# Performance work log

Hardware: AMD Instinct MI355X
Metric: run time of the kernel (lower is better)

Reference implementation:

```python
import jax, jax.numpy as jnp
import numpy as np
import math

B, NG, LS, E = 2, 8, 512, 1024
NH = 16
HD = E // NH
EPS = 1e-6


def rms_norm(x, w):
    xf = x.astype(jnp.float32)
    n = xf * jax.lax.rsqrt(jnp.mean(xf * xf, axis=-1, keepdims=True) + EPS)
    return n.astype(x.dtype) * w


def rotate(x):
    # pairs (a,b) -> (-b, a), matching view(...,-1,2).flip(-1); x[...,0]*=-1
    x2 = x.reshape(*x.shape[:-1], HD // 2, 2)
    out = jnp.stack([-x2[..., 1], x2[..., 0]], axis=-1)
    return out.reshape(x.shape)


def setup_inputs() -> dict:
    key = jax.random.key(0)
    k1, k2, k3 = jax.random.split(key, 3)
    x = jax.random.normal(k1, (B, NG, LS, E), dtype=jnp.float32)
    W_qkv = jax.random.normal(k2, (E, 3 * E), dtype=jnp.float32) * (1.0 / math.sqrt(E))
    ln_w = jnp.ones((E,), dtype=jnp.float32)
    W_proj = jax.random.normal(k3, (E, E), dtype=jnp.float32) * (1.0 / math.sqrt(E))
    return {"x": x, "W_qkv": W_qkv, "ln_w": ln_w, "W_proj": W_proj}


def reference(x, W_qkv, ln_w, W_proj):
    b, ng, ls, _ = x.shape
    qkv = jnp.einsum('bgsc,ce->bgse', x, W_qkv)  # fused QKV projection
    q, k, v = jnp.split(qkv, 3, axis=-1)
    # QK RMSNorm over full embedding dim (before head split)
    q = rms_norm(q, ln_w)
    k = rms_norm(k, ln_w)
    # [B, ng, nh, ls, hd]
    q = q.reshape(b, ng, ls, NH, HD).swapaxes(2, 3)
    k = k.reshape(b, ng, ls, NH, HD).swapaxes(2, 3)
    v = v.reshape(b, ng, ls, NH, HD).swapaxes(2, 3)
    # RoPE (repo's variant: angles duplicated across halves, adjacent-pair rotate)
    pos = 10000.0 ** ((-2.0 * jnp.arange(0, HD, 2, dtype=jnp.float32) - 1.0) / HD)
    token_seq = jnp.arange(ls, dtype=jnp.float32)[:, None] * pos[None, :]  # [ls, hd/2]
    rot = jnp.concatenate([token_seq, token_seq], axis=-1)  # [ls, hd]
    cos, sin = jnp.cos(rot), jnp.sin(rot)
    q = q * cos + rotate(q) * sin
    k = k * cos + rotate(k) * sin
    # causal attention, scale = 1/sqrt(head_dim) (muP=False)
    scale = 1.0 / math.sqrt(HD)
    scores = jnp.einsum('bgnqd,bgnkd->bgnqk', q, k) * scale
    causal = jnp.tril(jnp.ones((ls, ls), dtype=bool))
    scores = jnp.where(causal, scores, jnp.finfo(scores.dtype).min)
    att = jax.nn.softmax(scores, axis=-1)
    y = jnp.einsum('bgnqk,bgnkd->bgnqd', att, v)
    y = y.swapaxes(2, 3).reshape(b, ng, ls, E)
    y = jnp.einsum('bgse,ef->bgsf', y, W_proj)
    return y
```

## Files before the change

kernel.cpp:

```cpp
#include <hip/hip_runtime.h>

typedef unsigned short u16;
typedef unsigned int   u32;
typedef __attribute__((ext_vector_type(8))) short bf16x8;
typedef __attribute__((ext_vector_type(4))) float f32x4;

#define MFMA16(a,b,c) __builtin_amdgcn_mfma_f32_16x16x32_bf16((a),(b),(c),0,0,0)
#define GLD16(gp, lp) __builtin_amdgcn_global_load_lds((const __attribute__((address_space(1))) u32*)(gp), (__attribute__((address_space(3))) u32*)(lp), 16, 0, 0)

#define B_   2
#define NG_  8
#define LS_  512
#define E_   1024
#define NH_  16
#define HD_  64
#define NTOK 8192

__device__ __forceinline__ u16 f2bu(float f){
  u32 u = __builtin_bit_cast(u32, f);
  u32 r = u + 0x7FFFu + ((u >> 16) & 1u);
  return (u16)(r >> 16);
}
__device__ __forceinline__ float b2f(u16 h){
  u32 u = ((u32)h) << 16;
  return __builtin_bit_cast(float, u);
}
__device__ __forceinline__ u32 pk2(float lo, float hi){
  u32 r; asm("v_cvt_pk_bf16_f32 %0, %1, %2" : "=v"(r) : "v"(lo), "v"(hi)); return r;
}

__global__ __launch_bounds__(256) void k_conv_x(const float* __restrict__ x, u16* __restrict__ xb){
  int i = blockIdx.x * 256 + threadIdx.x;
  float4 v = ((const float4*)x)[i];
  ((ushort4*)xb)[i] = make_ushort4(f2bu(v.x), f2bu(v.y), f2bu(v.z), f2bu(v.w));
}

__global__ __launch_bounds__(256) void k_transpose(const float* __restrict__ W, u16* __restrict__ WT,
                                                   int Kd, int Nd){
  __shared__ float tile[32][33];
  int tx = threadIdx.x & 31, ty = threadIdx.x >> 5;
  int c0 = blockIdx.x * 32, r0 = blockIdx.y * 32;
  #pragma unroll
  for (int i = 0; i < 4; i++)
    tile[ty + i*8][tx] = W[(size_t)(r0 + ty + i*8) * Nd + c0 + tx];
  __syncthreads();
  #pragma unroll
  for (int i = 0; i < 4; i++)
    WT[(size_t)(c0 + ty + i*8) * Kd + r0 + tx] = f2bu(tile[tx][ty + i*8]);
}

__global__ __launch_bounds__(256) void k_rope_table(float* __restrict__ ct, float* __restrict__ st){
  int i = blockIdx.x * 256 + threadIdx.x;
  int s = i >> 6, d = i & 63, j = d & 31;
  float freq = powf(10000.f, -(4.f * (float)j + 1.f) / 64.f);
  float th = (float)s * freq;
  ct[i] = cosf(th);
  st[i] = sinf(th);
}

template <typename OutT, bool FUSE_VT>
__global__ __launch_bounds__(256, 2) void k_gemm_bt(const u16* __restrict__ A, const u16* __restrict__ Bt,
                                                    OutT* __restrict__ C, u16* __restrict__ vt,
                                                    int M, int N, int K){
  int nbn = N >> 7;
  int cpx = gridDim.x >> 3;
  int bid = (blockIdx.x & 7) * cpx + (blockIdx.x >> 3);
  int tm = bid / nbn, tn = bid % nbn;
  int tid = threadIdx.x;
  int w = tid >> 6, l = tid & 63;
  int lr = l & 15, lg = l >> 4;
  int wm = (w >> 1) * 64, wn = (w & 1) * 64;

  __shared__ u16 smem[2][2][128 * 64];

  const u16* Ab = A  + (size_t)(tm * 128) * K;
  const u16* Bb = Bt + (size_t)(tn * 128) * K;
  int NT = K >> 6;

  int srow0 = tid >> 3, ssl = tid & 7;
  auto stage = [&](int t, int s){
    int k0 = t << 6;
    #pragma unroll
    for (int q = 0; q < 4; q++){
      int row = q * 32 + srow0;
      int sc  = (ssl ^ (row & 7)) << 3;
      GLD16(Ab + (size_t)row * K + k0 + sc, &smem[s][0][q * 2048 + tid * 8]);
    }
    #pragma unroll
    for (int q = 0; q < 4; q++){
      int row = q * 32 + srow0;
      int sc  = (ssl ^ (row & 7)) << 3;
      GLD16(Bb + (size_t)row * K + k0 + sc, &smem[s][1][q * 2048 + tid * 8]);
    }
  };

  f32x4 acc[4][4] = {};

  stage(0, 0);
  stage(1, 1);
  asm volatile("s_waitcnt vmcnt(8)" ::: "memory");
  asm volatile("s_barrier" ::: "memory");

  for (int t = 0; t < NT; t++){
    int s = t & 1;
    const u16* As = smem[s][0];
    const u16* Bs = smem[s][1];
    bf16x8 bfr[4][2], afr[2][2];
    #pragma unroll
    for (int j = 0; j < 4; j++){
      int rb = wn + j * 16 + lr;
      #pragma unroll
      for (int kk = 0; kk < 2; kk++)
        bfr[j][kk] = *(const bf16x8*)&Bs[rb * 64 + ((kk * 32 + lg * 8) ^ ((rb & 7) << 3))];
    }
    #pragma unroll
    for (int i = 0; i < 2; i++){
      int ra = wm + i * 16 + lr;
      #pragma unroll
      for (int kk = 0; kk < 2; kk++)
        afr[i][kk] = *(const bf16x8*)&As[ra * 64 + ((kk * 32 + lg * 8) ^ ((ra & 7) << 3))];
    }
    __builtin_amdgcn_s_setprio(1);
    #pragma unroll
    for (int i = 0; i < 2; i++)
      #pragma unroll
      for (int j = 0; j < 4; j++){
        acc[i][j] = MFMA16(afr[i][0], bfr[j][0], acc[i][j]);
        acc[i][j] = MFMA16(afr[i][1], bfr[j][1], acc[i][j]);
      }
    __builtin_amdgcn_s_setprio(0);
    asm volatile("s_barrier" ::: "memory");
    #pragma unroll
    for (int i = 0; i < 2; i++){
      int ra = wm + (i + 2) * 16 + lr;
      #pragma unroll
      for (int kk = 0; kk < 2; kk++)
        afr[i][kk] = *(const bf16x8*)&As[ra * 64 + ((kk * 32 + lg * 8) ^ ((ra & 7) << 3))];
    }
    __builtin_amdgcn_s_setprio(1);
    #pragma unroll
    for (int i = 0; i < 2; i++)
      #pragma unroll
      for (int j = 0; j < 4; j++){
        acc[i + 2][j] = MFMA16(afr[i][0], bfr[j][0], acc[i + 2][j]);
        acc[i + 2][j] = MFMA16(afr[i][1], bfr[j][1], acc[i + 2][j]);
      }
    __builtin_amdgcn_s_setprio(0);
    asm volatile("s_barrier" ::: "memory");
    if (t + 2 < NT){
      stage(t + 2, s);
      asm volatile("s_waitcnt vmcnt(8)" ::: "memory");
      asm volatile("s_barrier" ::: "memory");
    } else if (t + 2 == NT){
      asm volatile("s_waitcnt vmcnt(0)" ::: "memory");
      asm volatile("s_barrier" ::: "memory");
    }
  }

  if constexpr (FUSE_VT){
    if (tn >= 16){
      int h  = (tn - 16) * 2 + (wn >> 6);
      int bg = tm >> 2;
      u16* vbase = vt + (size_t)(bg * 16 + h) * HD_ * LS_;
      #pragma unroll
      for (int i = 0; i < 4; i++){
        int s0 = (tm & 3) * 128 + wm + i * 16 + lg * 4;
        #pragma unroll
        for (int j = 0; j < 4; j++){
          int d = j * 16 + lr;
          ushort4 pk = make_ushort4(f2bu(acc[i][j][0]), f2bu(acc[i][j][1]),
                                    f2bu(acc[i][j][2]), f2bu(acc[i][j][3]));
          *(ushort4*)&vbase[(size_t)d * LS_ + s0] = pk;
        }
      }
      return;
    }
  }

  #pragma unroll
  for (int i = 0; i < 4; i++)
    #pragma unroll
    for (int j = 0; j < 4; j++)
      #pragma unroll
      for (int r = 0; r < 4; r++){
        int row = tm * 128 + wm + i * 16 + lg * 4 + r;
        int col = tn * 128 + wn + j * 16 + lr;
        float v = acc[i][j][r];
        if constexpr (sizeof(OutT) == 2) C[(size_t)row * N + col] = f2bu(v);
        else                             C[(size_t)row * N + col] = v;
      }
}

__global__ __launch_bounds__(256) void k_norm_rope(const u16* __restrict__ qkv, const float* __restrict__ lnw,
                                                   const float* __restrict__ ct, const float* __restrict__ st,
                                                   u16* __restrict__ qh, u16* __restrict__ kh){
  int tok = blockIdx.x;
  int t = threadIdx.x;
  int s = tok & (LS_ - 1);
  int bg = tok >> 9;
  const u16* row = qkv + (size_t)tok * 3072;
  int e0 = t * 4;

  ushort4 q4 = *(const ushort4*)&row[e0];
  ushort4 k4 = *(const ushort4*)&row[1024 + e0];
  float qf[4] = {b2f(q4.x), b2f(q4.y), b2f(q4.z), b2f(q4.w)};
  float kf[4] = {b2f(k4.x), b2f(k4.y), b2f(k4.z), b2f(k4.w)};

  float qss = 0.f, kss = 0.f;
  #pragma unroll
  for (int j = 0; j < 4; j++){ qss += qf[j]*qf[j]; kss += kf[j]*kf[j]; }
  #pragma unroll
  for (int o = 32; o; o >>= 1){ qss += __shfl_down(qss, o); kss += __shfl_down(kss, o); }
  __shared__ float redq[4], redk[4];
  if ((t & 63) == 0){ redq[t >> 6] = qss; redk[t >> 6] = kss; }
  __syncthreads();
  float qsum = redq[0] + redq[1] + redq[2] + redq[3];
  float ksum = redk[0] + redk[1] + redk[2] + redk[3];
  float qr = rsqrtf(qsum * (1.f / 1024.f) + 1e-6f);
  float kr = rsqrtf(ksum * (1.f / 1024.f) + 1e-6f);

  float qn[4], kn[4];
  #pragma unroll
  for (int j = 0; j < 4; j++){
    float wv = lnw[e0 + j];
    qn[j] = qf[j] * qr * wv;
    kn[j] = kf[j] * kr * wv;
  }
  int d0 = e0 & 63, h = e0 >> 6;
  const float* cr = ct + s * 64 + d0;
  const float* sr = st + s * 64 + d0;
  float qo[4], ko[4];
  #pragma unroll
  for (int p = 0; p < 4; p += 2){
    float c0 = cr[p], s0 = sr[p], c1 = cr[p+1], s1 = sr[p+1];
    qo[p]   = qn[p]   * c0 - qn[p+1] * s0;
    qo[p+1] = qn[p+1] * c1 + qn[p]   * s1;
    ko[p]   = kn[p]   * c0 - kn[p+1] * s0;
    ko[p+1] = kn[p+1] * c1 + kn[p]   * s1;
  }
  size_t oidx = (((size_t)bg * NH_ + h) * LS_ + s) * HD_ + d0;
  *(ushort4*)&qh[oidx] = make_ushort4(f2bu(qo[0]*0.125f), f2bu(qo[1]*0.125f), f2bu(qo[2]*0.125f), f2bu(qo[3]*0.125f));
  *(ushort4*)&kh[oidx] = make_ushort4(f2bu(ko[0]), f2bu(ko[1]), f2bu(ko[2]), f2bu(ko[3]));
}

__global__ __launch_bounds__(64) void k_attn(const u16* __restrict__ qh, const u16* __restrict__ kh,
                                             const u16* __restrict__ vt, u16* __restrict__ ytok){
  int bid = blockIdx.x;
  int head = bid & 255;
  int j = 15 - (bid >> 8);
  int l = threadIdx.x & 63;
  int lr = l & 15, lg = l >> 4;
  int q0 = j * 32;
  int ntw = (j >> 1) + 1;

  const u16* Qp = qh + (size_t)head * LS_ * HD_;
  const u16* Kp = kh + (size_t)head * LS_ * HD_;
  const u16* Vp = vt + (size_t)head * HD_ * LS_;
  int bg = head >> 4, h = head & 15;
  u16* Yb = ytok + (size_t)bg * LS_ * E_ + h * HD_;

  bf16x8 aq[2][2];
  #pragma unroll
  for (int mi = 0; mi < 2; mi++)
    #pragma unroll
    for (int kk = 0; kk < 2; kk++)
      aq[mi][kk] = *(const bf16x8*)&Qp[(q0 + mi*16 + lr) * 64 + kk * 32 + lg * 8];

  __shared__ u16 Pw[32 * 72];

  f32x4 o[2][4] = {};
  float mrun[2] = {-1e30f, -1e30f}, lrun[2] = {0.f, 0.f};

  bf16x8 kr[4][2];
  auto loadK = [&](int kv0){
    #pragma unroll
    for (int nk = 0; nk < 4; nk++){
      kr[nk][0] = *(const bf16x8*)&Kp[(kv0 + nk*16 + lr) * 64 + lg * 8];
      kr[nk][1] = *(const bf16x8*)&Kp[(kv0 + nk*16 + lr) * 64 + 32 + lg * 8];
    }
  };
  loadK(0);

  for (int tkv = 0; tkv < ntw; tkv++){
    int kv0 = tkv * 64;
    f32x4 sa[2][4] = {};
    __builtin_amdgcn_s_setprio(1);
    #pragma unroll
    for (int nk = 0; nk < 4; nk++)
      #pragma unroll
      for (int mi = 0; mi < 2; mi++){
        sa[mi][nk] = MFMA16(kr[nk][0], aq[mi][0], sa[mi][nk]);
        sa[mi][nk] = MFMA16(kr[nk][1], aq[mi][1], sa[mi][nk]);
      }
    __builtin_amdgcn_s_setprio(0);
    if (tkv + 1 < ntw) loadK(kv0 + 64);
    bf16x8 vr[4][2];
    #pragma unroll
    for (int nd = 0; nd < 4; nd++){
      vr[nd][0] = *(const bf16x8*)&Vp[(nd*16 + lr) * 512 + kv0 + lg * 8];
      vr[nd][1] = *(const bf16x8*)&Vp[(nd*16 + lr) * 512 + kv0 + 32 + lg * 8];
    }
    if (kv0 + 63 > q0){
      #pragma unroll
      for (int mi = 0; mi < 2; mi++){
        int qg = q0 + mi*16 + lr;
        #pragma unroll
        for (int nk = 0; nk < 4; nk++)
          #pragma unroll
          for (int r = 0; r < 4; r++){
            int kg = kv0 + nk*16 + lg*4 + r;
            if (kg > qg) sa[mi][nk][r] = -1e30f;
          }
      }
    }
    float pmax[2];
    #pragma unroll
    for (int mi = 0; mi < 2; mi++){
      float pm = sa[mi][0][0];
      #pragma unroll
      for (int nk = 0; nk < 4; nk++)
        #pragma unroll
        for (int r = 0; r < 4; r++) pm = fmaxf(pm, sa[mi][nk][r]);
      pm = fmaxf(pm, __shfl_xor(pm, 16));
      pm = fmaxf(pm, __shfl_xor(pm, 32));
      pmax[mi] = pm;
    }
    float dm = fmaxf(pmax[0] - mrun[0], pmax[1] - mrun[1]);
    if (!__all(dm <= 8.f)){
      float alpha[2];
      #pragma unroll
      for (int mi = 0; mi < 2; mi++){
        float mnew = fmaxf(mrun[mi], pmax[mi]);
        alpha[mi] = __expf(mrun[mi] - mnew);
        mrun[mi] = mnew;
        lrun[mi] *= alpha[mi];
      }
      #pragma unroll
      for (int r = 0; r < 4; r++){
        float a0 = __shfl(alpha[0], lg * 4 + r);
        float a1 = __shfl(alpha[1], lg * 4 + r);
        #pragma unroll
        for (int nd = 0; nd < 4; nd++){ o[0][nd][r] *= a0; o[1][nd][r] *= a1; }
      }
    }
    #pragma unroll
    for (int mi = 0; mi < 2; mi++){
      float psum = 0.f;
      #pragma unroll
      for (int nk = 0; nk < 4; nk++)
        #pragma unroll
        for (int r = 0; r < 4; r++){
          float pv = __expf(sa[mi][nk][r] - mrun[mi]);
          sa[mi][nk][r] = pv;
          psum += pv;
        }
      psum += __shfl_xor(psum, 16);
      psum += __shfl_xor(psum, 32);
      lrun[mi] += psum;
    }
    #pragma unroll
    for (int mi = 0; mi < 2; mi++)
      #pragma unroll
      for (int nk = 0; nk < 4; nk++){
        *(u32*)&Pw[(mi*16 + lr) * 72 + nk * 16 + lg * 4]     = pk2(sa[mi][nk][0], sa[mi][nk][1]);
        *(u32*)&Pw[(mi*16 + lr) * 72 + nk * 16 + lg * 4 + 2] = pk2(sa[mi][nk][2], sa[mi][nk][3]);
      }
    bf16x8 pa[2][2];
    #pragma unroll
    for (int mi = 0; mi < 2; mi++){
      pa[mi][0] = *(const bf16x8*)&Pw[(mi*16 + lr) * 72 + lg * 8];
      pa[mi][1] = *(const bf16x8*)&Pw[(mi*16 + lr) * 72 + 32 + lg * 8];
    }
    __builtin_amdgcn_s_setprio(1);
    #pragma unroll
    for (int nd = 0; nd < 4; nd++)
      #pragma unroll
      for (int mi = 0; mi < 2; mi++){
        o[mi][nd] = MFMA16(pa[mi][0], vr[nd][0], o[mi][nd]);
        o[mi][nd] = MFMA16(pa[mi][1], vr[nd][1], o[mi][nd]);
      }
    __builtin_amdgcn_s_setprio(0);
  }

  #pragma unroll
  for (int mi = 0; mi < 2; mi++){
    float linv = 1.f / lrun[mi];
    #pragma unroll
    for (int r = 0; r < 4; r++){
      float ir = __shfl(linv, lg * 4 + r);
      int qg = q0 + mi*16 + lg * 4 + r;
      #pragma unroll
      for (int nd = 0; nd < 4; nd++)
        Yb[(size_t)qg * E_ + nd * 16 + lr] = f2bu(o[mi][nd][r] * ir);
    }
  }
}

extern "C" void kernel_launch(void* const* d_in, const int* in_sizes, int n_in,
                              void* d_out, int out_size, void* d_ws, size_t ws_size,
                              hipStream_t stream){
  const float* x     = (const float*)d_in[0];
  const float* Wqkv  = (const float*)d_in[1];
  const float* lnw   = (const float*)d_in[2];
  const float* Wproj = (const float*)d_in[3];
  float* out = (float*)d_out;

  u16* p = (u16*)d_ws;
  u16* xb     = p; p += (size_t)NTOK * E_;
  u16* wqkvT  = p; p += (size_t)3 * E_ * E_;
  u16* wprojT = p; p += (size_t)E_ * E_;
  u16* qkv    = p; p += (size_t)NTOK * 3 * E_;
  u16* qhp    = p; p += (size_t)NTOK * E_;
  u16* khp    = p; p += (size_t)NTOK * E_;
  u16* vtp    = p; p += (size_t)NTOK * E_;
  float* ct = (float*)p;
  float* st = ct + LS_ * HD_;

  k_conv_x<<<8192, 256, 0, stream>>>(x, xb);
  k_transpose<<<dim3(96, 32), 256, 0, stream>>>(Wqkv, wqkvT, 1024, 3072);
  k_transpose<<<dim3(32, 32), 256, 0, stream>>>(Wproj, wprojT, 1024, 1024);
  k_rope_table<<<128, 256, 0, stream>>>(ct, st);
  k_gemm_bt<u16, true><<<64 * 24, 256, 0, stream>>>(xb, wqkvT, qkv, vtp, NTOK, 3 * E_, E_);
  k_norm_rope<<<NTOK, 256, 0, stream>>>(qkv, lnw, ct, st, qhp, khp);
  k_attn<<<4096, 64, 0, stream>>>(qhp, khp, vtp, xb);
  k_gemm_bt<float, false><<<64 * 8, 256, 0, stream>>>(xb, wprojT, out, nullptr, NTOK, E_, E_);
}
```

Before: 157.3 us.

## Enlarge GEMM tile to 256x128 with 8 waves and quadrant-interleaved MFMA schedule

The GEMM kernel moves from 128x128 tiles with 4 waves to 256x128 tiles with 8 waves (512 threads, one block per CU). Each wave computes a 64x64 sub-tile in four quadrant phases separated by barriers, and the next-stage global-to-LDS prefetch is issued before the last quadrant's MFMAs. The intent is to raise operand reuse per tile and overlap loads with compute. The cost is more barriers and lower occupancy, and the projection GEMM gets only 256 blocks, which may underfill the CUs.

```diff
diff --git a/kernel.cpp b/kernel.cpp
--- a/kernel.cpp
+++ b/kernel.cpp
@@ -59,7 +59,7 @@
 }
 
 template <typename OutT, bool FUSE_VT>
-__global__ __launch_bounds__(256, 2) void k_gemm_bt(const u16* __restrict__ A, const u16* __restrict__ Bt,
+__global__ __launch_bounds__(512, 1) void k_gemm_bt(const u16* __restrict__ A, const u16* __restrict__ Bt,
                                                     OutT* __restrict__ C, u16* __restrict__ vt,
                                                     int M, int N, int K){
   int nbn = N >> 7;
@@ -69,28 +69,29 @@
   int tid = threadIdx.x;
   int w = tid >> 6, l = tid & 63;
   int lr = l & 15, lg = l >> 4;
-  int wm = (w >> 1) * 64, wn = (w & 1) * 64;
-
-  __shared__ u16 smem[2][2][128 * 64];
-
-  const u16* Ab = A  + (size_t)(tm * 128) * K;
+  int wr = w >> 1, wc = w & 1;
+
+  __shared__ u16 sA[2][256 * 64];
+  __shared__ u16 sB[2][128 * 64];
+
+  const u16* Ab = A  + (size_t)(tm * 256) * K;
   const u16* Bb = Bt + (size_t)(tn * 128) * K;
   int NT = K >> 6;
 
-  int srow0 = tid >> 3, ssl = tid & 7;
+  int rowt = tid >> 3, slot = tid & 7;
   auto stage = [&](int t, int s){
     int k0 = t << 6;
     #pragma unroll
     for (int q = 0; q < 4; q++){
-      int row = q * 32 + srow0;
-      int sc  = (ssl ^ (row & 7)) << 3;
-      GLD16(Ab + (size_t)row * K + k0 + sc, &smem[s][0][q * 2048 + tid * 8]);
-    }
-    #pragma unroll
-    for (int q = 0; q < 4; q++){
-      int row = q * 32 + srow0;
-      int sc  = (ssl ^ (row & 7)) << 3;
-      GLD16(Bb + (size_t)row * K + k0 + sc, &smem[s][1][q * 2048 + tid * 8]);
+      int row = q * 64 + rowt;
+      int sc  = (slot ^ (row & 7)) << 3;
+      GLD16(Ab + (size_t)row * K + k0 + sc, &sA[s][q * 4096 + tid * 8]);
+    }
+    #pragma unroll
+    for (int q = 0; q < 2; q++){
+      int row = q * 64 + rowt;
+      int sc  = (slot ^ (row & 7)) << 3;
+      GLD16(Bb + (size_t)row * K + k0 + sc, &sB[s][q * 4096 + tid * 8]);
     }
   };
 
@@ -98,78 +99,109 @@
 
   stage(0, 0);
   stage(1, 1);
-  asm volatile("s_waitcnt vmcnt(8)" ::: "memory");
+  asm volatile("s_waitcnt vmcnt(6)" ::: "memory");
   asm volatile("s_barrier" ::: "memory");
 
   for (int t = 0; t < NT; t++){
-    int s = t & 1;
-    const u16* As = smem[s][0];
-    const u16* Bs = smem[s][1];
-    bf16x8 bfr[4][2], afr[2][2];
-    #pragma unroll
-    for (int j = 0; j < 4; j++){
-      int rb = wn + j * 16 + lr;
+    const u16* As = sA[t & 1];
+    const u16* Bs = sB[t & 1];
+    bf16x8 af[4][2], bf[4][2];
+
+    #pragma unroll
+    for (int m = 0; m < 2; m++){
+      int ra = wr * 64 + m * 16 + lr;
       #pragma unroll
       for (int kk = 0; kk < 2; kk++)
-        bfr[j][kk] = *(const bf16x8*)&Bs[rb * 64 + ((kk * 32 + lg * 8) ^ ((rb & 7) << 3))];
-    }
-    #pragma unroll
-    for (int i = 0; i < 2; i++){
-      int ra = wm + i * 16 + lr;
+        af[m][kk] = *(const bf16x8*)&As[ra * 64 + ((kk * 32 + lg * 8) ^ ((ra & 7) << 3))];
+    }
+    #pragma unroll
+    for (int n = 0; n < 2; n++){
+      int rb = wc * 64 + n * 16 + lr;
       #pragma unroll
       for (int kk = 0; kk < 2; kk++)
-        afr[i][kk] = *(const bf16x8*)&As[ra * 64 + ((kk * 32 + lg * 8) ^ ((ra & 7) << 3))];
-    }
-    __builtin_amdgcn_s_setprio(1);
-    #pragma unroll
-    for (int i = 0; i < 2; i++)
-      #pragma unroll
-      for (int j = 0; j < 4; j++){
-        acc[i][j] = MFMA16(afr[i][0], bfr[j][0], acc[i][j]);
-        acc[i][j] = MFMA16(afr[i][1], bfr[j][1], acc[i][j]);
-      }
-    __builtin_amdgcn_s_setprio(0);
-    asm volatile("s_barrier" ::: "memory");
-    #pragma unroll
-    for (int i = 0; i < 2; i++){
-      int ra = wm + (i + 2) * 16 + lr;
+        bf[n][kk] = *(const bf16x8*)&Bs[rb * 64 + ((kk * 32 + lg * 8) ^ ((rb & 7) << 3))];
+    }
+    asm volatile("s_barrier" ::: "memory");
+    asm volatile("s_waitcnt lgkmcnt(0)" ::: "memory");
+    __builtin_amdgcn_s_setprio(1);
+    #pragma unroll
+    for (int m = 0; m < 2; m++)
+      #pragma unroll
+      for (int n = 0; n < 2; n++){
+        acc[m][n] = MFMA16(af[m][0], bf[n][0], acc[m][n]);
+        acc[m][n] = MFMA16(af[m][1], bf[n][1], acc[m][n]);
+      }
+    __builtin_amdgcn_s_setprio(0);
+    asm volatile("s_barrier" ::: "memory");
+
+    #pragma unroll
+    for (int m = 2; m < 4; m++){
+      int ra = wr * 64 + m * 16 + lr;
       #pragma unroll
       for (int kk = 0; kk < 2; kk++)
-        afr[i][kk] = *(const bf16x8*)&As[ra * 64 + ((kk * 32 + lg * 8) ^ ((ra & 7) << 3))];
-    }
-    __builtin_amdgcn_s_setprio(1);
-    #pragma unroll
-    for (int i = 0; i < 2; i++)
-      #pragma unroll
-      for (int j = 0; j < 4; j++){
-        acc[i + 2][j] = MFMA16(afr[i][0], bfr[j][0], acc[i + 2][j]);
-        acc[i + 2][j] = MFMA16(afr[i][1], bfr[j][1], acc[i + 2][j]);
-      }
-    __builtin_amdgcn_s_setprio(0);
-    asm volatile("s_barrier" ::: "memory");
-    if (t + 2 < NT){
-      stage(t + 2, s);
-      asm volatile("s_waitcnt vmcnt(8)" ::: "memory");
-      asm volatile("s_barrier" ::: "memory");
-    } else if (t + 2 == NT){
-      asm volatile("s_waitcnt vmcnt(0)" ::: "memory");
-      asm volatile("s_barrier" ::: "memory");
-    }
+        af[m][kk] = *(const bf16x8*)&As[ra * 64 + ((kk * 32 + lg * 8) ^ ((ra & 7) << 3))];
+    }
+    asm volatile("s_barrier" ::: "memory");
+    asm volatile("s_waitcnt lgkmcnt(0)" ::: "memory");
+    __builtin_amdgcn_s_setprio(1);
+    #pragma unroll
+    for (int m = 2; m < 4; m++)
+      #pragma unroll
+      for (int n = 0; n < 2; n++){
+        acc[m][n] = MFMA16(af[m][0], bf[n][0], acc[m][n]);
+        acc[m][n] = MFMA16(af[m][1], bf[n][1], acc[m][n]);
+      }
+    __builtin_amdgcn_s_setprio(0);
+    asm volatile("s_barrier" ::: "memory");
+
+    #pragma unroll
+    for (int n = 2; n < 4; n++){
+      int rb = wc * 64 + n * 16 + lr;
+      #pragma unroll
+      for (int kk = 0; kk < 2; kk++)
+        bf[n][kk] = *(const bf16x8*)&Bs[rb * 64 + ((kk * 32 + lg * 8) ^ ((rb & 7) << 3))];
+    }
+    asm volatile("s_barrier" ::: "memory");
+    asm volatile("s_waitcnt lgkmcnt(0)" ::: "memory");
+    __builtin_amdgcn_s_setprio(1);
+    #pragma unroll
+    for (int m = 0; m < 2; m++)
+      #pragma unroll
+      for (int n = 2; n < 4; n++){
+        acc[m][n] = MFMA16(af[m][0], bf[n][0], acc[m][n]);
+        acc[m][n] = MFMA16(af[m][1], bf[n][1], acc[m][n]);
+      }
+    __builtin_amdgcn_s_setprio(0);
+    asm volatile("s_barrier" ::: "memory");
+
+    if (t + 2 < NT) stage(t + 2, t & 1);
+    __builtin_amdgcn_s_setprio(1);
+    #pragma unroll
+    for (int m = 2; m < 4; m++)
+      #pragma unroll
+      for (int n = 2; n < 4; n++){
+        acc[m][n] = MFMA16(af[m][0], bf[n][0], acc[m][n]);
+        acc[m][n] = MFMA16(af[m][1], bf[n][1], acc[m][n]);
+      }
+    __builtin_amdgcn_s_setprio(0);
+    if (t + 2 < NT)       asm volatile("s_waitcnt vmcnt(6)" ::: "memory");
+    else if (t + 2 == NT) asm volatile("s_waitcnt vmcnt(0)" ::: "memory");
+    asm volatile("s_barrier" ::: "memory");
   }
 
   if constexpr (FUSE_VT){
     if (tn >= 16){
-      int h  = (tn - 16) * 2 + (wn >> 6);
-      int bg = tm >> 2;
-      u16* vbase = vt + (size_t)(bg * 16 + h) * HD_ * LS_;
-      #pragma unroll
-      for (int i = 0; i < 4; i++){
-        int s0 = (tm & 3) * 128 + wm + i * 16 + lg * 4;
+      int h = (tn - 16) * 2 + wc;
+      int g = tm >> 1;
+      u16* vbase = vt + (size_t)(g * 16 + h) * HD_ * LS_;
+      #pragma unroll
+      for (int m = 0; m < 4; m++){
+        int s0 = (tm & 1) * 256 + wr * 64 + m * 16 + lg * 4;
         #pragma unroll
-        for (int j = 0; j < 4; j++){
-          int d = j * 16 + lr;
-          ushort4 pk = make_ushort4(f2bu(acc[i][j][0]), f2bu(acc[i][j][1]),
-                                    f2bu(acc[i][j][2]), f2bu(acc[i][j][3]));
+        for (int n = 0; n < 4; n++){
+          int d = n * 16 + lr;
+          ushort4 pk = make_ushort4(f2bu(acc[m][n][0]), f2bu(acc[m][n][1]),
+                                    f2bu(acc[m][n][2]), f2bu(acc[m][n][3]));
           *(ushort4*)&vbase[(size_t)d * LS_ + s0] = pk;
         }
       }
@@ -178,14 +210,14 @@
   }
 
   #pragma unroll
-  for (int i = 0; i < 4; i++)
-    #pragma unroll
-    for (int j = 0; j < 4; j++)
+  for (int m = 0; m < 4; m++)
+    #pragma unroll
+    for (int n = 0; n < 4; n++)
       #pragma unroll
       for (int r = 0; r < 4; r++){
-        int row = tm * 128 + wm + i * 16 + lg * 4 + r;
-        int col = tn * 128 + wn + j * 16 + lr;
-        float v = acc[i][j][r];
+        int row = tm * 256 + wr * 64 + m * 16 + lg * 4 + r;
+        int col = tn * 128 + wc * 64 + n * 16 + lr;
+        float v = acc[m][n][r];
         if constexpr (sizeof(OutT) == 2) C[(size_t)row * N + col] = f2bu(v);
         else                             C[(size_t)row * N + col] = v;
       }
@@ -420,8 +452,8 @@
   k_transpose<<<dim3(96, 32), 256, 0, stream>>>(Wqkv, wqkvT, 1024, 3072);
   k_transpose<<<dim3(32, 32), 256, 0, stream>>>(Wproj, wprojT, 1024, 1024);
   k_rope_table<<<128, 256, 0, stream>>>(ct, st);
-  k_gemm_bt<u16, true><<<64 * 24, 256, 0, stream>>>(xb, wqkvT, qkv, vtp, NTOK, 3 * E_, E_);
+  k_gemm_bt<u16, true><<<768, 512, 0, stream>>>(xb, wqkvT, qkv, vtp, NTOK, 3 * E_, E_);
   k_norm_rope<<<NTOK, 256, 0, stream>>>(qkv, lnw, ct, st, qhp, khp);
   k_attn<<<4096, 64, 0, stream>>>(qhp, khp, vtp, xb);
-  k_gemm_bt<float, false><<<64 * 8, 256, 0, stream>>>(xb, wprojT, out, nullptr, NTOK, E_, E_);
-}
+  k_gemm_bt<float, false><<<256, 512, 0, stream>>>(xb, wprojT, out, nullptr, NTOK, E_, E_);
+}
```

New measurement: 174.4 us. 10.9% more time.
